# Performance work log

Measured on AMD Instinct MI355X. Metric: run time of the kernel, lower is better.

## Reference

```python
import jax, jax.numpy as jnp
import numpy as np

B, S, L, D, H, DH, DFF, V = 16, 512, 12, 512, 8, 64, 2048, 631
MAX_KLEN = 1024  # tgt_len + mem_len


def _ln(x, g, b, eps=1e-5):
    m = x.mean(-1, keepdims=True)
    v = ((x - m) ** 2).mean(-1, keepdims=True)
    return (x - m) / jnp.sqrt(v + eps) * g + b


def _rot_half(x):
    # interleaved pair rotation: (x0,x1,x2,x3,..) -> (-x1,x0,-x3,x2,..)
    xe = x[..., ::2]
    xo = x[..., 1::2]
    return jnp.stack((-xo, xe), axis=-1).reshape(x.shape)


def _sin_cos(seq_len, d_head):
    inv_freq = 1.0 / 10000.0 ** (jnp.arange(0, d_head, 2, dtype=jnp.float32) / d_head)
    t = jnp.arange(seq_len, dtype=jnp.float32)[:, None] * inv_freq[None, :]
    sin = jnp.repeat(jnp.sin(t), 2, axis=-1)  # (S, DH)
    cos = jnp.repeat(jnp.cos(t), 2, axis=-1)
    return sin, cos


def setup_inputs() -> dict:
    key = jax.random.key(0)
    ks = jax.random.split(key, 12)
    std = 0.02
    data = jax.random.randint(ks[0], (B, S), 0, V)
    emb = jax.random.normal(ks[1], (V, D), jnp.float32) * std
    pos = jax.random.normal(ks[2], (MAX_KLEN, D), jnp.float32) * std
    Wq = jax.random.normal(ks[3], (L, D, H * DH), jnp.float32) * std
    Wkv = jax.random.normal(ks[4], (L, D, 2 * H * DH), jnp.float32) * std
    Wo = jax.random.normal(ks[5], (L, H * DH, D), jnp.float32) * std
    W1 = jax.random.normal(ks[6], (L, D, DFF), jnp.float32) * std
    b1 = jnp.zeros((L, DFF), jnp.float32)
    W2 = jax.random.normal(ks[7], (L, DFF, D), jnp.float32) * std
    b2 = jnp.zeros((L, D), jnp.float32)
    ln1_g = jnp.ones((L, D), jnp.float32)
    ln1_b = jnp.zeros((L, D), jnp.float32)
    ln2_g = jnp.ones((L, D), jnp.float32)
    ln2_b = jnp.zeros((L, D), jnp.float32)
    out_b = jnp.zeros((V,), jnp.float32)
    return dict(data=data, emb=emb, pos=pos, Wq=Wq, Wkv=Wkv, Wo=Wo,
                W1=W1, b1=b1, W2=W2, b2=b2,
                ln1_g=ln1_g, ln1_b=ln1_b, ln2_g=ln2_g, ln2_b=ln2_b, out_b=out_b)


def reference(data, emb, pos, Wq, Wkv, Wo, W1, b1, W2, b2,
              ln1_g, ln1_b, ln2_g, ln2_b, out_b):
    sin, cos = _sin_cos(S, DH)
    sin = sin[None, :, None, :]  # (1,S,1,DH) broadcast over (B,S,H,DH)
    cos = cos[None, :, None, :]
    causal = jnp.triu(jnp.ones((S, S), bool), 1)
    scale = 1.0 / jnp.sqrt(jnp.float32(DH))

    h = emb[data] + pos[:S][None]  # (B,S,D)
    for l in range(L):
        q = (h @ Wq[l]).reshape(B, S, H, DH)
        kv = h @ Wkv[l]
        k = kv[..., :H * DH].reshape(B, S, H, DH)
        v = kv[..., H * DH:].reshape(B, S, H, DH)
        q = q * cos + _rot_half(q) * sin
        k = k * cos + _rot_half(k) * sin
        sc = jnp.einsum('bqhd,bkhd->bhqk', q, k) * scale
        sc = jnp.where(causal[None, None], -jnp.inf, sc)
        p = jax.nn.softmax(sc, axis=-1)
        av = jnp.einsum('bhqk,bkhd->bqhd', p, v).reshape(B, S, H * DH)
        h = _ln(h + av @ Wo[l], ln1_g[l], ln1_b[l])
        ff = jax.nn.relu(h @ W1[l] + b1[l]) @ W2[l] + b2[l]
        h = _ln(h + ff, ln2_g[l], ln2_b[l])
    # tied output projection: out_layer.weight = word_emb.weight, plus bias
    return h @ emb.T + out_b
```

## Files before the change

kernel.cpp:

```cpp
#include <hip/hip_runtime.h>
#include <hip/hip_bf16.h>

typedef __hip_bfloat16 bf16;
typedef __attribute__((ext_vector_type(8))) short short8;
typedef __attribute__((ext_vector_type(4))) float f32x4;

static constexpr int Bz = 16, Sq = 512, Lw = 12, Dm = 512, Hh = 8, DFFd = 2048, Vv = 631;
static constexpr int Mtok = Bz * Sq;
static constexpr int VPAD = 640;
static constexpr int QKS = 1024;

__device__ __forceinline__ bf16 f2b(float x) { return __float2bfloat16(x); }
__device__ __forceinline__ float bfu(unsigned short s) {
    union { unsigned u; float f; } c; c.u = (unsigned)s << 16; return c.f;
}

__device__ __forceinline__ f32x4 z4() { f32x4 v; v[0]=0.f; v[1]=0.f; v[2]=0.f; v[3]=0.f; return v; }

__device__ __forceinline__ void gload_lds16(const bf16* g, bf16* l) {
    __builtin_amdgcn_global_load_lds(
        (const __attribute__((address_space(1))) unsigned int*)(g),
        (__attribute__((address_space(3))) unsigned int*)(l),
        16, 0, 0);
}

__global__ void k_sincos(float* __restrict__ cosT, float* __restrict__ sinT) {
    int i = blockIdx.x * 256 + threadIdx.x;
    int s = i >> 5, f = i & 31;
    float inv = powf(10000.0f, -(float)(2 * f) / 64.0f);
    float t = (float)s * inv;
    sinT[i] = sinf(t);
    cosT[i] = cosf(t);
}

__global__ void k_embconv(const float* __restrict__ emb, bf16* __restrict__ embT) {
    int i = blockIdx.x * 256 + threadIdx.x;
    int n = i >> 9;
    embT[i] = (n < Vv) ? f2b(emb[i]) : f2b(0.0f);
}

__global__ void k_embed(const int* __restrict__ data, const float* __restrict__ emb,
                        const float* __restrict__ pos, bf16* __restrict__ hb) {
    int tok = blockIdx.x;
    int id = data[tok];
    int s = tok & (Sq - 1);
    for (int d = threadIdx.x; d < Dm; d += 256) {
        float v = emb[id * Dm + d] + pos[s * Dm + d];
        hb[(size_t)tok * Dm + d] = f2b(v);
    }
}

__global__ void k_wtrans(const float* __restrict__ src, bf16* __restrict__ dst,
                         int K, int N, long long sStride, long long dStride) {
    src += (long long)blockIdx.z * sStride;
    dst += (long long)blockIdx.z * dStride;
    __shared__ float tile[32][33];
    int k0 = blockIdx.y * 32, n0 = blockIdx.x * 32;
    int tx = threadIdx.x & 31, ty = threadIdx.x >> 5;
    #pragma unroll
    for (int r = ty; r < 32; r += 8) tile[r][tx] = src[(size_t)(k0 + r) * N + n0 + tx];
    __syncthreads();
    #pragma unroll
    for (int r = ty; r < 32; r += 8) dst[(size_t)(n0 + r) * K + k0 + tx] = f2b(tile[tx][r]);
}

template<int EPI, int BM>
__global__ __launch_bounds__(512) void k_gemmW(const bf16* __restrict__ A, const bf16* __restrict__ Bt,
                                               void* __restrict__ Cout, void* __restrict__ Cout2,
                                               const float* __restrict__ bias,
                                               const float* __restrict__ cosT, const float* __restrict__ sinT,
                                               int M, int N, int K, int ldA, int ldB) {
    constexpr int PA  = BM / 128;
    constexpr int NI  = BM / 64;
    constexpr int WRS = BM / 4;
    extern __shared__ __align__(16) char smem[];
    bf16* lAbase = (bf16*)smem;
    bf16* lBbase = (bf16*)(smem + 3 * BM * 32 * 2);

    const int t = threadIdx.x;
    const int lane = t & 63;
    const int wave = t >> 6;
    const int wr = wave >> 1, wc = wave & 1;
    const int l15 = lane & 15, l4 = lane >> 4;

    const int gx = gridDim.x, gy = gridDim.y;
    const int nwg = gx * gy * gridDim.z;
    const int cpx = nwg >> 3;
    int lin = (blockIdx.z * gy + blockIdx.y) * gx + blockIdx.x;
    lin = (lin & 7) * cpx + (lin >> 3);
    const int bn = lin % gx;
    const int rem = lin / gx;
    const int bm = rem % gy;
    const int bz = rem / gy;

    const bf16* Ab = A + (size_t)(bm * BM) * ldA + (size_t)bz * K;
    const bf16* Bb = Bt + (size_t)(bn * 128) * ldB + (size_t)bz * K;

    int soffA[PA], soffB0;
    #pragma unroll
    for (int p = 0; p < PA; p++) {
        int q = p * 512 + t, r = q >> 2, s = q & 3;
        soffA[p] = r * ldA + ((s ^ ((r >> 1) & 3)) << 3);
    }
    {
        int r = t >> 2, s = t & 3;
        soffB0 = r * ldB + ((s ^ ((r >> 1) & 3)) << 3);
    }

    f32x4 acc[NI][4];
    #pragma unroll
    for (int i = 0; i < NI; i++)
        #pragma unroll
        for (int j = 0; j < 4; j++) acc[i][j] = z4();

    auto STAGE = [&](int buf, int kt) {
        const int k0 = kt << 5;
        bf16* la = lAbase + buf * (BM * 32);
        bf16* lb = lBbase + buf * (128 * 32);
        #pragma unroll
        for (int p = 0; p < PA; p++)
            gload_lds16(Ab + (size_t)soffA[p] + k0, &la[(p * 512 + t) * 8]);
        gload_lds16(Bb + (size_t)soffB0 + k0, &lb[t * 8]);
    };

    auto COMPUTE = [&](int buf) {
        const char* la = (const char*)(lAbase + buf * (BM * 32));
        const char* lb = (const char*)(lBbase + buf * (128 * 32));
        short8 af[NI], bfr[4];
        #pragma unroll
        for (int i = 0; i < NI; i++) {
            int row = wr * WRS + i * 16 + l15;
            af[i] = *(const short8*)(la + row * 64 + (((l4 ^ (row >> 1)) & 3) << 4));
        }
        #pragma unroll
        for (int j = 0; j < 4; j++) {
            int row = wc * 64 + j * 16 + l15;
            bfr[j] = *(const short8*)(lb + row * 64 + (((l4 ^ (row >> 1)) & 3) << 4));
        }
        #pragma unroll
        for (int i = 0; i < NI; i++)
            #pragma unroll
            for (int j = 0; j < 4; j++)
                acc[i][j] = __builtin_amdgcn_mfma_f32_16x16x32_bf16(af[i], bfr[j], acc[i][j], 0, 0, 0);
    };

    const int nk = K >> 5;
    STAGE(0, 0);
    STAGE(1, 1);
    int kt = 0;
    for (; kt < nk - 1; ++kt) {
        if constexpr (PA == 2) asm volatile("s_waitcnt vmcnt(3)" ::: "memory");
        else                   asm volatile("s_waitcnt vmcnt(2)" ::: "memory");
        __builtin_amdgcn_s_barrier();
        if (kt + 2 < nk) STAGE((kt + 2) % 3, kt + 2);
        __builtin_amdgcn_s_setprio(1);
        COMPUTE(kt % 3);
        __builtin_amdgcn_s_setprio(0);
    }
    asm volatile("s_waitcnt vmcnt(0)" ::: "memory");
    __builtin_amdgcn_s_barrier();
    __builtin_amdgcn_s_setprio(1);
    COMPUTE(kt % 3);
    __builtin_amdgcn_s_setprio(0);

    #pragma unroll
    for (int i = 0; i < NI; i++) {
        #pragma unroll
        for (int j = 0; j < 4; j++) {
            const int col = bn * 128 + wc * 64 + j * 16 + l15;
            const int row0 = bm * BM + wr * WRS + i * 16 + l4 * 4;
            if (EPI == 4 && col >= 1024) {
                int h = (col - 1024) >> 6, d = (col - 1024) & 63;
                int b = row0 >> 9, s0 = row0 & 511;
                bf16 pk[4];
                #pragma unroll
                for (int r = 0; r < 4; r++) pk[r] = f2b(acc[i][j][r]);
                *(ushort4*)&((bf16*)Cout2)[((size_t)(b * 8 + h) * 64 + d) * 512 + s0] =
                    *(const ushort4*)pk;
                continue;
            }
            #pragma unroll
            for (int r = 0; r < 4; r++) {
                int row = row0 + r;
                float v = acc[i][j][r];
                if (EPI == 1) {
                    bf16* Co = (bf16*)(bz ? Cout2 : Cout);
                    Co[(size_t)row * N + col] = f2b(v);
                } else if (EPI == 2) {
                    v += bias[col];
                    v = v > 0.f ? v : 0.f;
                    ((bf16*)Cout)[(size_t)row * N + col] = f2b(v);
                } else if (EPI == 3) {
                    if (col < Vv) ((float*)Cout)[(size_t)row * Vv + col] = v + bias[col];
                } else {
                    float p = __shfl_xor(v, 1, 64);
                    int srow = row & (Sq - 1);
                    int f = (col >> 1) & 31;
                    float cc = cosT[srow * 32 + f], sn = sinT[srow * 32 + f];
                    float o = (col & 1) ? (v * cc + p * sn) : (v * cc - p * sn);
                    if (col < 512) o *= 0.125f;
                    ((bf16*)Cout)[(size_t)row * QKS + col] = f2b(o);
                }
            }
        }
    }
}

__global__ __launch_bounds__(512) void k_attn(const bf16* __restrict__ qkv,
                                              const bf16* __restrict__ vt, bf16* __restrict__ av) {
    __shared__ __align__(16) bf16 lK[2][64][80];
    __shared__ __align__(16) bf16 lV[2][64][80];
    __shared__ __align__(16) bf16 lP[8][16][88];
    const int tq = blockIdx.x, bh = blockIdx.y;
    const int b = bh >> 3, h = bh & 7;
    const int t = threadIdx.x, lane = t & 63, w = t >> 6;
    const int l15 = lane & 15, l4 = lane >> 4;
    const int q0 = tq * 128;
    const int rowb = q0 + w * 16;

    short8 qf[2];
    {
        const bf16* qr = qkv + (size_t)(b * Sq + rowb + l15) * QKS + h * 64 + l4 * 8;
        qf[0] = *(const short8*)qr;
        qf[1] = *(const short8*)(qr + 32);
    }
    f32x4 o[4];
    #pragma unroll
    for (int j = 0; j < 4; j++) o[j] = z4();
    float mrow[4] = {-1e30f, -1e30f, -1e30f, -1e30f};
    float ssum[4] = {0.f, 0.f, 0.f, 0.f};

    const int nk = (q0 >> 6) + 2;
    const int sr = t >> 3, scc = (t & 7) * 8;
    const bf16* gK = qkv + (size_t)(b * Sq + sr) * QKS + 512 + h * 64 + scc;
    const bf16* gV = vt + (size_t)(bh * 64 + sr) * 512 + scc;
    uint4 rK = *(const uint4*)gK;
    uint4 rV = *(const uint4*)gV;

    for (int kt = 0; kt < nk; ++kt) {
        const int buf = kt & 1;
        const int kv0 = kt * 64;
        uint4 nK, nV;
        if (kt + 1 < nk) {
            nK = *(const uint4*)(gK + (size_t)(kt + 1) * 64 * QKS);
            nV = *(const uint4*)(gV + (size_t)(kt + 1) * 64);
        }
        *(uint4*)&lK[buf][sr][scc] = rK;
        *(uint4*)&lV[buf][sr][scc] = rV;
        asm volatile("s_waitcnt lgkmcnt(0)" ::: "memory");
        __builtin_amdgcn_s_barrier();
        __builtin_amdgcn_sched_barrier(0);

        if (kv0 <= rowb + 15) {
            f32x4 sc[4];
            #pragma unroll
            for (int j = 0; j < 4; j++) sc[j] = z4();
            #pragma unroll
            for (int j = 0; j < 4; j++)
                #pragma unroll
                for (int ks = 0; ks < 2; ks++) {
                    short8 kf = *(const short8*)&lK[buf][j * 16 + l15][ks * 32 + l4 * 8];
                    sc[j] = __builtin_amdgcn_mfma_f32_16x16x32_bf16(qf[ks], kf, sc[j], 0, 0, 0);
                }
            if (kv0 + 63 > rowb) {
                #pragma unroll
                for (int j = 0; j < 4; j++)
                    #pragma unroll
                    for (int r = 0; r < 4; r++)
                        if (kv0 + j * 16 + l15 > rowb + l4 * 4 + r) sc[j][r] = -1e30f;
            }
            float corr[4];
            #pragma unroll
            for (int r = 0; r < 4; r++) {
                float m_ = fmaxf(fmaxf(sc[0][r], sc[1][r]), fmaxf(sc[2][r], sc[3][r]));
                #pragma unroll
                for (int d = 1; d < 16; d <<= 1) m_ = fmaxf(m_, __shfl_xor(m_, d, 64));
                float mo = mrow[r];
                float mn = fmaxf(mo, m_);
                mrow[r] = mn;
                corr[r] = __expf(mo - mn);
            }
            float p[4][4];
            #pragma unroll
            for (int j = 0; j < 4; j++)
                #pragma unroll
                for (int r = 0; r < 4; r++)
                    p[j][r] = __expf(sc[j][r] - mrow[r]);
            #pragma unroll
            for (int r = 0; r < 4; r++)
                ssum[r] = ssum[r] * corr[r] + p[0][r] + p[1][r] + p[2][r] + p[3][r];
            #pragma unroll
            for (int j = 0; j < 4; j++)
                #pragma unroll
                for (int r = 0; r < 4; r++)
                    lP[w][l4 * 4 + r][j * 16 + l15] = f2b(p[j][r]);
            #pragma unroll
            for (int j = 0; j < 4; j++) {
                o[j][0] *= corr[0]; o[j][1] *= corr[1]; o[j][2] *= corr[2]; o[j][3] *= corr[3];
            }
            #pragma unroll
            for (int ks = 0; ks < 2; ks++) {
                short8 pa = *(const short8*)&lP[w][l15][ks * 32 + l4 * 8];
                #pragma unroll
                for (int j = 0; j < 4; j++) {
                    short8 vb = *(const short8*)&lV[buf][j * 16 + l15][ks * 32 + l4 * 8];
                    o[j] = __builtin_amdgcn_mfma_f32_16x16x32_bf16(pa, vb, o[j], 0, 0, 0);
                }
            }
        }
        rK = nK; rV = nV;
    }
    #pragma unroll
    for (int r = 0; r < 4; r++) {
        float s = ssum[r];
        #pragma unroll
        for (int d = 1; d < 16; d <<= 1) s += __shfl_xor(s, d, 64);
        ssum[r] = 1.f / s;
    }
    #pragma unroll
    for (int j = 0; j < 4; j++)
        #pragma unroll
        for (int r = 0; r < 4; r++)
            av[(size_t)(b * Sq + rowb + l4 * 4 + r) * 512 + h * 64 + j * 16 + l15] = f2b(o[j][r] * ssum[r]);
}

template<bool ADDB>
__global__ __launch_bounds__(256) void k_addln(bf16* __restrict__ hb,
                                               const bf16* __restrict__ d1, const bf16* __restrict__ d2,
                                               const float* __restrict__ bias,
                                               const float* __restrict__ gamma, const float* __restrict__ beta) {
    const int lane = threadIdx.x & 63, w = threadIdx.x >> 6;
    const int row = blockIdx.x * 4 + w;
    const size_t base = (size_t)row * Dm + lane * 8;
    float v[8];
    short8 h8 = *(const short8*)&hb[base];
    short8 a8 = *(const short8*)&d1[base];
    short8 b8 = *(const short8*)&d2[base];
    #pragma unroll
    for (int k = 0; k < 8; k++)
        v[k] = bfu((unsigned short)h8[k]) + bfu((unsigned short)a8[k]) + bfu((unsigned short)b8[k]);
    if (ADDB) {
        float4 bb0 = *(const float4*)&bias[lane * 8];
        float4 bb1 = *(const float4*)&bias[lane * 8 + 4];
        v[0] += bb0.x; v[1] += bb0.y; v[2] += bb0.z; v[3] += bb0.w;
        v[4] += bb1.x; v[5] += bb1.y; v[6] += bb1.z; v[7] += bb1.w;
    }
    float s = 0.f, sq = 0.f;
    #pragma unroll
    for (int k = 0; k < 8; k++) { s += v[k]; sq += v[k] * v[k]; }
    #pragma unroll
    for (int m = 1; m < 64; m <<= 1) { s += __shfl_xor(s, m, 64); sq += __shfl_xor(sq, m, 64); }
    float mean = s * (1.f / Dm);
    float var = sq * (1.f / Dm) - mean * mean;
    float inv = rsqrtf(var + 1e-5f);
    float4 g0 = *(const float4*)&gamma[lane * 8];
    float4 g1 = *(const float4*)&gamma[lane * 8 + 4];
    float4 e0 = *(const float4*)&beta[lane * 8];
    float4 e1 = *(const float4*)&beta[lane * 8 + 4];
    float gs[8] = {g0.x, g0.y, g0.z, g0.w, g1.x, g1.y, g1.z, g1.w};
    float es[8] = {e0.x, e0.y, e0.z, e0.w, e1.x, e1.y, e1.z, e1.w};
    short8 ob;
    #pragma unroll
    for (int k = 0; k < 8; k++) {
        float ov = (v[k] - mean) * inv * gs[k] + es[k];
        ob[k] = (short)__bfloat16_as_ushort(f2b(ov));
    }
    *(short8*)&hb[base] = ob;
}

extern "C" void kernel_launch(void* const* d_in, const int* in_sizes, int n_in,
                              void* d_out, int out_size, void* d_ws, size_t ws_size,
                              hipStream_t stream) {
    const int*   data = (const int*)d_in[0];
    const float* emb  = (const float*)d_in[1];
    const float* pos  = (const float*)d_in[2];
    const float* Wq   = (const float*)d_in[3];
    const float* Wkv  = (const float*)d_in[4];
    const float* Wo   = (const float*)d_in[5];
    const float* W1   = (const float*)d_in[6];
    const float* b1   = (const float*)d_in[7];
    const float* W2   = (const float*)d_in[8];
    const float* b2   = (const float*)d_in[9];
    const float* ln1g = (const float*)d_in[10];
    const float* ln1b = (const float*)d_in[11];
    const float* ln2g = (const float*)d_in[12];
    const float* ln2b = (const float*)d_in[13];
    const float* outb = (const float*)d_in[14];
    float* out = (float*)d_out;
    char* ws = (char*)d_ws;

    const int WL256 = 3 * (256 * 32 + 128 * 32) * 2;
    const int WL128 = 3 * (128 * 32 + 128 * 32) * 2;
    (void)hipFuncSetAttribute((const void*)&k_gemmW<1, 128>, hipFuncAttributeMaxDynamicSharedMemorySize, WL128);
    (void)hipFuncSetAttribute((const void*)&k_gemmW<2, 256>, hipFuncAttributeMaxDynamicSharedMemorySize, WL256);
    (void)hipFuncSetAttribute((const void*)&k_gemmW<3, 128>, hipFuncAttributeMaxDynamicSharedMemorySize, WL128);
    (void)hipFuncSetAttribute((const void*)&k_gemmW<4, 128>, hipFuncAttributeMaxDynamicSharedMemorySize, WL128);

    size_t off = 0;
    auto take = [&](size_t bytes) { size_t r = off; off += (bytes + 255) & ~(size_t)255; return r; };
    bf16*  hb    = (bf16*)(ws + take((size_t)Mtok * Dm * 2));
    bf16*  qkvbf = (bf16*)(ws + take((size_t)Mtok * QKS * 2));
    bf16*  vtb   = (bf16*)(ws + take((size_t)Mtok * Dm * 2));
    bf16*  avb   = (bf16*)(ws + take((size_t)Mtok * Dm * 2));
    bf16*  tmpb  = (bf16*)(ws + take((size_t)Mtok * Dm * 2));
    bf16*  tmp2b = (bf16*)(ws + take((size_t)Mtok * Dm * 2));
    bf16*  ff1   = (bf16*)(ws + take((size_t)Mtok * DFFd * 2));
    float* cosT  = (float*)(ws + take((size_t)Sq * 32 * 4));
    float* sinT  = (float*)(ws + take((size_t)Sq * 32 * 4));
    bf16*  embT  = (bf16*)(ws + take((size_t)VPAD * Dm * 2));

    const size_t ofsQKV = 0;
    const size_t ofsO   = ofsQKV + (size_t)1536 * 512;
    const size_t ofsW1  = ofsO + (size_t)512 * 512;
    const size_t ofsW2  = ofsW1 + (size_t)512 * 2048;
    const size_t SLABE  = ofsW2 + (size_t)2048 * 512;

    bf16* wT = (bf16*)(ws + off);
    size_t remain = (ws_size > off) ? (ws_size - off) : 0;
    bool upfront = remain >= SLABE * 12 * 2;

    k_sincos<<<(Sq * 32) / 256, 256, 0, stream>>>(cosT, sinT);
    k_embconv<<<(VPAD * Dm) / 256, 256, 0, stream>>>(emb, embT);
    k_embed<<<Mtok, 256, 0, stream>>>(data, emb, pos, hb);

    if (upfront) {
        k_wtrans<<<dim3(16, 16, 12), 256, 0, stream>>>(Wq,  wT + ofsQKV,             512, 512,  (long long)512 * 512,  (long long)SLABE);
        k_wtrans<<<dim3(32, 16, 12), 256, 0, stream>>>(Wkv, wT + ofsQKV + 512 * 512, 512, 1024, (long long)512 * 1024, (long long)SLABE);
        k_wtrans<<<dim3(16, 16, 12), 256, 0, stream>>>(Wo,  wT + ofsO,  512, 512,  (long long)512 * 512,  (long long)SLABE);
        k_wtrans<<<dim3(64, 16, 12), 256, 0, stream>>>(W1,  wT + ofsW1, 512, 2048, (long long)512 * 2048, (long long)SLABE);
        k_wtrans<<<dim3(16, 64, 12), 256, 0, stream>>>(W2,  wT + ofsW2, 2048, 512, (long long)2048 * 512, (long long)SLABE);
    }

    for (int l = 0; l < Lw; l++) {
        bf16* slab = wT + (upfront ? (size_t)l * SLABE : 0);
        if (!upfront) {
            k_wtrans<<<dim3(16, 16, 1), 256, 0, stream>>>(Wq  + (size_t)l * 512 * 512,  slab + ofsQKV,             512, 512,  0, 0);
            k_wtrans<<<dim3(32, 16, 1), 256, 0, stream>>>(Wkv + (size_t)l * 512 * 1024, slab + ofsQKV + 512 * 512, 512, 1024, 0, 0);
            k_wtrans<<<dim3(16, 16, 1), 256, 0, stream>>>(Wo  + (size_t)l * 512 * 512,  slab + ofsO,  512, 512,  0, 0);
            k_wtrans<<<dim3(64, 16, 1), 256, 0, stream>>>(W1  + (size_t)l * 512 * 2048, slab + ofsW1, 512, 2048, 0, 0);
            k_wtrans<<<dim3(16, 64, 1), 256, 0, stream>>>(W2  + (size_t)l * 2048 * 512, slab + ofsW2, 2048, 512, 0, 0);
        }
        k_gemmW<4, 128><<<dim3(12, 64, 1), 512, WL128, stream>>>(hb, slab + ofsQKV, qkvbf, vtb, nullptr, cosT, sinT,
                                                                 Mtok, 1536, 512, 512, 512);
        k_attn<<<dim3(4, 128), 512, 0, stream>>>(qkvbf, vtb, avb);
        k_gemmW<1, 128><<<dim3(4, 64, 2), 512, WL128, stream>>>(avb, slab + ofsO, tmpb, tmp2b, nullptr, nullptr, nullptr,
                                                                Mtok, 512, 256, 512, 512);
        k_addln<false><<<Mtok / 4, 256, 0, stream>>>(hb, tmpb, tmp2b, nullptr,
                                                     ln1g + (size_t)l * Dm, ln1b + (size_t)l * Dm);
        k_gemmW<2, 256><<<dim3(16, 32, 1), 512, WL256, stream>>>(hb, slab + ofsW1, ff1, nullptr, b1 + (size_t)l * DFFd,
                                                                 nullptr, nullptr, Mtok, 2048, 512, 512, 512);
        k_gemmW<1, 128><<<dim3(4, 64, 2), 512, WL128, stream>>>(ff1, slab + ofsW2, tmpb, tmp2b, nullptr, nullptr, nullptr,
                                                                Mtok, 512, 1024, 2048, 2048);
        k_addln<true><<<Mtok / 4, 256, 0, stream>>>(hb, tmpb, tmp2b, b2 + (size_t)l * Dm,
                                                    ln2g + (size_t)l * Dm, ln2b + (size_t)l * Dm);
    }
    k_gemmW<3, 128><<<dim3(5, 64, 1), 512, WL128, stream>>>(hb, embT, out, nullptr, outb, nullptr, nullptr,
                                                            Mtok, VPAD, 512, 512, 512);
}
```

Measured before the change: 1.510 ms.

## Deepen GEMM LDS pipeline to five stages for BM=128 and fuse sincos into embconv

For the 128-row GEMM variants the LDS ring buffer grows from three to five stages. Loads are now issued four tiles ahead, with matching vmcnt waits and an explicit three-step drain at the end, to hide more global-load latency. The sincos table computation is folded into the embedding conversion kernel, which removes one launch. The extra LDS (80KB per block) may cut occupancy, and the hand-written vmcnt counts depend on the exact number of loads per stage.

```diff
diff --git a/kernel.cpp b/kernel.cpp
--- a/kernel.cpp
+++ b/kernel.cpp
@@ -24,19 +24,18 @@
         16, 0, 0);
 }
 
-__global__ void k_sincos(float* __restrict__ cosT, float* __restrict__ sinT) {
-    int i = blockIdx.x * 256 + threadIdx.x;
-    int s = i >> 5, f = i & 31;
-    float inv = powf(10000.0f, -(float)(2 * f) / 64.0f);
-    float t = (float)s * inv;
-    sinT[i] = sinf(t);
-    cosT[i] = cosf(t);
-}
-
-__global__ void k_embconv(const float* __restrict__ emb, bf16* __restrict__ embT) {
+__global__ void k_embconv(const float* __restrict__ emb, bf16* __restrict__ embT,
+                          float* __restrict__ cosT, float* __restrict__ sinT) {
     int i = blockIdx.x * 256 + threadIdx.x;
     int n = i >> 9;
     embT[i] = (n < Vv) ? f2b(emb[i]) : f2b(0.0f);
+    if (i < Sq * 32) {
+        int s = i >> 5, f = i & 31;
+        float inv = powf(10000.0f, -(float)(2 * f) / 64.0f);
+        float t = (float)s * inv;
+        sinT[i] = sinf(t);
+        cosT[i] = cosf(t);
+    }
 }
 
 __global__ void k_embed(const int* __restrict__ data, const float* __restrict__ emb,
@@ -73,9 +72,10 @@
     constexpr int PA  = BM / 128;
     constexpr int NI  = BM / 64;
     constexpr int WRS = BM / 4;
+    constexpr int RNG = (BM == 128) ? 5 : 3;
     extern __shared__ __align__(16) char smem[];
     bf16* lAbase = (bf16*)smem;
-    bf16* lBbase = (bf16*)(smem + 3 * BM * 32 * 2);
+    bf16* lBbase = (bf16*)(smem + RNG * BM * 32 * 2);
 
     const int t = threadIdx.x;
     const int lane = t & 63;
@@ -145,23 +145,44 @@
     };
 
     const int nk = K >> 5;
-    STAGE(0, 0);
-    STAGE(1, 1);
-    int kt = 0;
-    for (; kt < nk - 1; ++kt) {
-        if constexpr (PA == 2) asm volatile("s_waitcnt vmcnt(3)" ::: "memory");
-        else                   asm volatile("s_waitcnt vmcnt(2)" ::: "memory");
+    #pragma unroll
+    for (int p = 0; p < RNG - 1; ++p) STAGE(p, p);
+
+    if constexpr (BM == 128) {
+        int kt = 0;
+        for (; kt < nk - 3; ++kt) {
+            asm volatile("s_waitcnt vmcnt(6)" ::: "memory");
+            __builtin_amdgcn_s_barrier();
+            if (kt + 4 < nk) STAGE((kt + 4) % 5, kt + 4);
+            __builtin_amdgcn_s_setprio(1);
+            COMPUTE(kt % 5);
+            __builtin_amdgcn_s_setprio(0);
+        }
+        asm volatile("s_waitcnt vmcnt(4)" ::: "memory");
         __builtin_amdgcn_s_barrier();
-        if (kt + 2 < nk) STAGE((kt + 2) % 3, kt + 2);
+        __builtin_amdgcn_s_setprio(1); COMPUTE((nk - 3) % 5); __builtin_amdgcn_s_setprio(0);
+        asm volatile("s_waitcnt vmcnt(2)" ::: "memory");
+        __builtin_amdgcn_s_barrier();
+        __builtin_amdgcn_s_setprio(1); COMPUTE((nk - 2) % 5); __builtin_amdgcn_s_setprio(0);
+        asm volatile("s_waitcnt vmcnt(0)" ::: "memory");
+        __builtin_amdgcn_s_barrier();
+        __builtin_amdgcn_s_setprio(1); COMPUTE((nk - 1) % 5); __builtin_amdgcn_s_setprio(0);
+    } else {
+        int kt = 0;
+        for (; kt < nk - 1; ++kt) {
+            asm volatile("s_waitcnt vmcnt(3)" ::: "memory");
+            __builtin_amdgcn_s_barrier();
+            if (kt + 2 < nk) STAGE((kt + 2) % 3, kt + 2);
+            __builtin_amdgcn_s_setprio(1);
+            COMPUTE(kt % 3);
+            __builtin_amdgcn_s_setprio(0);
+        }
+        asm volatile("s_waitcnt vmcnt(0)" ::: "memory");
+        __builtin_amdgcn_s_barrier();
         __builtin_amdgcn_s_setprio(1);
         COMPUTE(kt % 3);
         __builtin_amdgcn_s_setprio(0);
     }
-    asm volatile("s_waitcnt vmcnt(0)" ::: "memory");
-    __builtin_amdgcn_s_barrier();
-    __builtin_amdgcn_s_setprio(1);
-    COMPUTE(kt % 3);
-    __builtin_amdgcn_s_setprio(0);
 
     #pragma unroll
     for (int i = 0; i < NI; i++) {
@@ -390,7 +411,7 @@
     char* ws = (char*)d_ws;
 
     const int WL256 = 3 * (256 * 32 + 128 * 32) * 2;
-    const int WL128 = 3 * (128 * 32 + 128 * 32) * 2;
+    const int WL128 = 5 * (128 * 32 + 128 * 32) * 2;
     (void)hipFuncSetAttribute((const void*)&k_gemmW<1, 128>, hipFuncAttributeMaxDynamicSharedMemorySize, WL128);
     (void)hipFuncSetAttribute((const void*)&k_gemmW<2, 256>, hipFuncAttributeMaxDynamicSharedMemorySize, WL256);
     (void)hipFuncSetAttribute((const void*)&k_gemmW<3, 128>, hipFuncAttributeMaxDynamicSharedMemorySize, WL128);
@@ -419,8 +440,7 @@
     size_t remain = (ws_size > off) ? (ws_size - off) : 0;
     bool upfront = remain >= SLABE * 12 * 2;
 
-    k_sincos<<<(Sq * 32) / 256, 256, 0, stream>>>(cosT, sinT);
-    k_embconv<<<(VPAD * Dm) / 256, 256, 0, stream>>>(emb, embT);
+    k_embconv<<<(VPAD * Dm) / 256, 256, 0, stream>>>(emb, embT, cosT, sinT);
     k_embed<<<Mtok, 256, 0, stream>>>(data, emb, pos, hb);
 
     if (upfront) {
```

New measurement: 1.550 ms. 1.03x slower.
